# Kernel tuning notes

Hardware: AMD Instinct MI355X
Metric: run time of the kernel (lower is better)

The kernel has to match this reference:

```python
import jax, jax.numpy as jnp
import numpy as np

N, K, D = 16384, 32, 256
NEG_SLOPE = 0.01  # torch F.leaky_relu default


def setup_inputs() -> dict:
    key = jax.random.key(0)
    k1, k2, k3, k4 = jax.random.split(key, 4)
    scale = 1.0 / np.sqrt(D)
    return {
        "target": jax.random.normal(k1, (N, D), dtype=jnp.float32),
        "middle": jax.random.normal(k2, (N, K, D), dtype=jnp.float32),
        "W": jax.random.normal(k3, (D, D), dtype=jnp.float32) * scale,
        "b": jnp.zeros((D,), dtype=jnp.float32),
        "a_w": jax.random.normal(k4, (1, D), dtype=jnp.float32) * scale,
        "a_b": jnp.zeros((1,), dtype=jnp.float32),
    }


def reference(target, middle, W, b, a_w, a_b):
    # attention_weight applied to both target and middle (bias added to each,
    # matching the torch code which sums two Linear outputs)
    pt = target @ W.T + b              # [N, D]
    pm = middle @ W.T + b              # [N, K, D]
    h = pt[:, None, :] + pm            # [N, K, D]
    # a_weight: D -> 1
    score = h @ a_w.T + a_b            # [N, K, 1]
    score = jax.nn.leaky_relu(score, negative_slope=NEG_SLOPE)
    coef = jax.nn.softmax(score, axis=-2)   # softmax over neighbor dim K
    neighbor_feature = jnp.sum(coef * middle, axis=-2)  # [N, D]
    return neighbor_feature
```

## Files before the change

### kernel.cpp

```cpp
#include <hip/hip_runtime.h>

#define N_ 16384
#define K_ 32
#define D_ 256
#define NEG_SLOPE 0.01f

__global__ __launch_bounds__(256) void prep_kernel(
    const float* __restrict__ W, const float* __restrict__ b,
    const float* __restrict__ a_w, const float* __restrict__ a_b,
    float* __restrict__ ws) {
  const int t = threadIdx.x;
  const int i = blockIdx.x;
  float acc = 0.f;
#pragma unroll
  for (int j = 0; j < 8; ++j) {
    const int d = i * 8 + j;
    acc += a_w[d] * W[d * D_ + t];
  }
  atomicAdd(&ws[t], acc);

  if (i == 0) {
    float s = b[t] * a_w[t];
#pragma unroll
    for (int off = 1; off < 64; off <<= 1) s += __shfl_xor(s, off);
    __shared__ float sp[4];
    if ((t & 63) == 0) sp[t >> 6] = s;
    __syncthreads();
    if (t == 0)
      atomicAdd(&ws[D_], 2.f * (sp[0] + sp[1] + sp[2] + sp[3]) + a_b[0]);
  }
}

__global__ __launch_bounds__(256, 2) void attn_agg_kernel(
    const float* __restrict__ target, const float* __restrict__ middle,
    const float* __restrict__ ws, float* __restrict__ out) {
  const int t = threadIdx.x;
  const int w = t >> 6;
  const int l = t & 63;
  const int n = blockIdx.x * 4 + w;

  const float4* m4p = (const float4*)(middle + (size_t)n * K_ * D_);
  const float4 vv = ((const float4*)ws)[l];
  const float cadd = ws[D_];
  const float4 tg = ((const float4*)(target + (size_t)n * D_))[l];

  float4 m[K_];
#pragma unroll
  for (int j = 0; j < K_; ++j) m[j] = m4p[j * 64 + l];

  float pd[16];
#pragma unroll
  for (int j = 0; j < 16; ++j) {
    float d = m[j].x * vv.x + m[j].y * vv.y + m[j].z * vv.z + m[j].w * vv.w;
    d += __shfl_xor(d, 32);
    pd[j] = d;
  }
#pragma unroll
  for (int j = 16; j < 32; ++j) {
    float d = m[j].x * vv.x + m[j].y * vv.y + m[j].z * vv.z + m[j].w * vv.w;
    d += __shfl_xor(d, 32);
    pd[j - 16] = (l & 32) ? d : pd[j - 16];
  }
#pragma unroll
  for (int i = 0; i < 16; ++i) pd[i] += __shfl_xor(pd[i], 16);
#pragma unroll
  for (int i = 0; i < 8; ++i) pd[i] = (l & 16) ? pd[i + 8] : pd[i];
#pragma unroll
  for (int i = 0; i < 8; ++i) pd[i] += __shfl_xor(pd[i], 8);
#pragma unroll
  for (int i = 0; i < 4; ++i) pd[i] = (l & 8) ? pd[i + 4] : pd[i];
#pragma unroll
  for (int i = 0; i < 4; ++i) pd[i] += __shfl_xor(pd[i], 4);
#pragma unroll
  for (int i = 0; i < 2; ++i) pd[i] = (l & 4) ? pd[i + 2] : pd[i];
#pragma unroll
  for (int i = 0; i < 2; ++i) pd[i] += __shfl_xor(pd[i], 2);
  pd[0] = (l & 2) ? pd[1] : pd[0];
  pd[0] += __shfl_xor(pd[0], 1);

  float tp = tg.x * vv.x + tg.y * vv.y + tg.z * vv.z + tg.w * vv.w;
  tp += __shfl_xor(tp, 32);
  tp += __shfl_xor(tp, 16);
  tp += __shfl_xor(tp, 8);
  tp += __shfl_xor(tp, 4);
  tp += __shfl_xor(tp, 2);
  tp += __shfl_xor(tp, 1);

  float sc = pd[0] + tp + cadd;
  sc = sc > 0.f ? sc : NEG_SLOPE * sc;
  float mx = sc;
  mx = fmaxf(mx, __shfl_xor(mx, 32));
  mx = fmaxf(mx, __shfl_xor(mx, 16));
  mx = fmaxf(mx, __shfl_xor(mx, 8));
  mx = fmaxf(mx, __shfl_xor(mx, 4));
  mx = fmaxf(mx, __shfl_xor(mx, 2));
  mx = fmaxf(mx, __shfl_xor(mx, 1));
  const float ex = __expf(sc - mx);
  float sm = ex;
  sm += __shfl_xor(sm, 32);
  sm += __shfl_xor(sm, 16);
  sm += __shfl_xor(sm, 8);
  sm += __shfl_xor(sm, 4);
  sm += __shfl_xor(sm, 2);
  sm += __shfl_xor(sm, 1);
  const float coef = 2.f * ex / sm;

  float4 acc = make_float4(0.f, 0.f, 0.f, 0.f);
#pragma unroll
  for (int j = 0; j < K_; ++j) {
    const float cf =
        __int_as_float(__builtin_amdgcn_readlane(__float_as_int(coef), 2 * j));
    acc.x += cf * m[j].x;
    acc.y += cf * m[j].y;
    acc.z += cf * m[j].z;
    acc.w += cf * m[j].w;
  }
  ((float4*)(out + (size_t)n * D_))[l] = acc;
}

extern "C" void kernel_launch(void* const* d_in, const int* in_sizes, int n_in,
                              void* d_out, int out_size, void* d_ws, size_t ws_size,
                              hipStream_t stream) {
  const float* target = (const float*)d_in[0];
  const float* middle = (const float*)d_in[1];
  const float* W      = (const float*)d_in[2];
  const float* b      = (const float*)d_in[3];
  const float* a_w    = (const float*)d_in[4];
  const float* a_b    = (const float*)d_in[5];
  float* out = (float*)d_out;
  float* ws  = (float*)d_ws;

  hipMemsetAsync(ws, 0, (D_ + 1) * sizeof(float), stream);
  prep_kernel<<<32, 256, 0, stream>>>(W, b, a_w, a_b, ws);
  attn_agg_kernel<<<N_ / 4, 256, 0, stream>>>(target, middle, ws, out);
}
```

Measured before the change: 127.0 us.

## Split each node across eight waves by feature slice with shared-memory score reduction

```diff
diff --git a/kernel.cpp b/kernel.cpp
--- a/kernel.cpp
+++ b/kernel.cpp
@@ -31,91 +31,94 @@
   }
 }
 
-__global__ __launch_bounds__(256, 2) void attn_agg_kernel(
+__global__ __launch_bounds__(512, 8) void attn_agg_kernel(
     const float* __restrict__ target, const float* __restrict__ middle,
     const float* __restrict__ ws, float* __restrict__ out) {
+  __shared__ float sdot_part[8][K_];
+  __shared__ float stgt[8];
+
   const int t = threadIdx.x;
-  const int w = t >> 6;
+  const int kg = t >> 6;
   const int l = t & 63;
-  const int n = blockIdx.x * 4 + w;
+  const int rg = l >> 3;
+  const int c = l & 7;
+  const int n = blockIdx.x;
 
-  const float4* m4p = (const float4*)(middle + (size_t)n * K_ * D_);
-  const float4 vv = ((const float4*)ws)[l];
+  const float* mbase = middle + (size_t)n * K_ * D_ + kg * 32 + c * 4;
+
+  float4 m[4];
+#pragma unroll
+  for (int j = 0; j < 4; ++j)
+    m[j] = *(const float4*)(mbase + (size_t)(8 * j + rg) * D_);
+
+  const float4 vv = *(const float4*)(ws + kg * 32 + c * 4);
   const float cadd = ws[D_];
-  const float4 tg = ((const float4*)(target + (size_t)n * D_))[l];
+  const float4 tg = *(const float4*)(target + (size_t)n * D_ + kg * 32 + c * 4);
 
-  float4 m[K_];
+  float pd[4];
 #pragma unroll
-  for (int j = 0; j < K_; ++j) m[j] = m4p[j * 64 + l];
-
-  float pd[16];
+  for (int j = 0; j < 4; ++j)
+    pd[j] = m[j].x * vv.x + m[j].y * vv.y + m[j].z * vv.z + m[j].w * vv.w;
 #pragma unroll
-  for (int j = 0; j < 16; ++j) {
-    float d = m[j].x * vv.x + m[j].y * vv.y + m[j].z * vv.z + m[j].w * vv.w;
-    d += __shfl_xor(d, 32);
-    pd[j] = d;
+  for (int j = 0; j < 4; ++j) {
+    pd[j] += __shfl_xor(pd[j], 1);
+    pd[j] += __shfl_xor(pd[j], 2);
+    pd[j] += __shfl_xor(pd[j], 4);
   }
+  if (c == 0) {
 #pragma unroll
-  for (int j = 16; j < 32; ++j) {
-    float d = m[j].x * vv.x + m[j].y * vv.y + m[j].z * vv.z + m[j].w * vv.w;
-    d += __shfl_xor(d, 32);
-    pd[j - 16] = (l & 32) ? d : pd[j - 16];
+    for (int j = 0; j < 4; ++j) sdot_part[kg][8 * j + rg] = pd[j];
   }
-#pragma unroll
-  for (int i = 0; i < 16; ++i) pd[i] += __shfl_xor(pd[i], 16);
-#pragma unroll
-  for (int i = 0; i < 8; ++i) pd[i] = (l & 16) ? pd[i + 8] : pd[i];
-#pragma unroll
-  for (int i = 0; i < 8; ++i) pd[i] += __shfl_xor(pd[i], 8);
-#pragma unroll
-  for (int i = 0; i < 4; ++i) pd[i] = (l & 8) ? pd[i + 4] : pd[i];
-#pragma unroll
-  for (int i = 0; i < 4; ++i) pd[i] += __shfl_xor(pd[i], 4);
-#pragma unroll
-  for (int i = 0; i < 2; ++i) pd[i] = (l & 4) ? pd[i + 2] : pd[i];
-#pragma unroll
-  for (int i = 0; i < 2; ++i) pd[i] += __shfl_xor(pd[i], 2);
-  pd[0] = (l & 2) ? pd[1] : pd[0];
-  pd[0] += __shfl_xor(pd[0], 1);
 
   float tp = tg.x * vv.x + tg.y * vv.y + tg.z * vv.z + tg.w * vv.w;
-  tp += __shfl_xor(tp, 32);
-  tp += __shfl_xor(tp, 16);
-  tp += __shfl_xor(tp, 8);
+  tp += __shfl_xor(tp, 1);
+  tp += __shfl_xor(tp, 2);
   tp += __shfl_xor(tp, 4);
-  tp += __shfl_xor(tp, 2);
-  tp += __shfl_xor(tp, 1);
+  if (l == 0) stgt[kg] = tp;
 
-  float sc = pd[0] + tp + cadd;
-  sc = sc > 0.f ? sc : NEG_SLOPE * sc;
+  __syncthreads();
+
+  const int k2 = l & 31;
+  float sd = cadd;
+#pragma unroll
+  for (int w = 0; w < 8; ++w) sd += sdot_part[w][k2];
+#pragma unroll
+  for (int w = 0; w < 8; ++w) sd += stgt[w];
+
+  float sc = sd > 0.f ? sd : NEG_SLOPE * sd;
   float mx = sc;
-  mx = fmaxf(mx, __shfl_xor(mx, 32));
+  mx = fmaxf(mx, __shfl_xor(mx, 1));
+  mx = fmaxf(mx, __shfl_xor(mx, 2));
+  mx = fmaxf(mx, __shfl_xor(mx, 4));
+  mx = fmaxf(mx, __shfl_xor(mx, 8));
   mx = fmaxf(mx, __shfl_xor(mx, 16));
-  mx = fmaxf(mx, __shfl_xor(mx, 8));
-  mx = fmaxf(mx, __shfl_xor(mx, 4));
-  mx = fmaxf(mx, __shfl_xor(mx, 2));
-  mx = fmaxf(mx, __shfl_xor(mx, 1));
   const float ex = __expf(sc - mx);
   float sm = ex;
-  sm += __shfl_xor(sm, 32);
+  sm += __shfl_xor(sm, 1);
+  sm += __shfl_xor(sm, 2);
+  sm += __shfl_xor(sm, 4);
+  sm += __shfl_xor(sm, 8);
   sm += __shfl_xor(sm, 16);
-  sm += __shfl_xor(sm, 8);
-  sm += __shfl_xor(sm, 4);
-  sm += __shfl_xor(sm, 2);
-  sm += __shfl_xor(sm, 1);
-  const float coef = 2.f * ex / sm;
+  const float coef = ex / sm;
 
   float4 acc = make_float4(0.f, 0.f, 0.f, 0.f);
 #pragma unroll
-  for (int j = 0; j < K_; ++j) {
-    const float cf =
-        __int_as_float(__builtin_amdgcn_readlane(__float_as_int(coef), 2 * j));
+  for (int j = 0; j < 4; ++j) {
+    const float cf = __shfl(coef, 8 * j + rg, 64);
     acc.x += cf * m[j].x;
     acc.y += cf * m[j].y;
     acc.z += cf * m[j].z;
     acc.w += cf * m[j].w;
   }
-  ((float4*)(out + (size_t)n * D_))[l] = acc;
+#pragma unroll
+  for (int off = 8; off <= 32; off <<= 1) {
+    acc.x += __shfl_xor(acc.x, off);
+    acc.y += __shfl_xor(acc.y, off);
+    acc.z += __shfl_xor(acc.z, off);
+    acc.w += __shfl_xor(acc.w, off);
+  }
+  if (rg == 0)
+    *(float4*)(out + (size_t)n * D_ + kg * 32 + c * 4) = acc;
 }
 
 extern "C" void kernel_launch(void* const* d_in, const int* in_sizes, int n_in,
@@ -132,5 +135,5 @@
 
   hipMemsetAsync(ws, 0, (D_ + 1) * sizeof(float), stream);
   prep_kernel<<<32, 256, 0, stream>>>(W, b, a_w, a_b, ws);
-  attn_agg_kernel<<<N_ / 4, 256, 0, stream>>>(target, middle, ws, out);
+  attn_agg_kernel<<<N_, 512, 0, stream>>>(target, middle, ws, out);
 }
```

Result: faster. 111.5 us (-12.2%).
